# Performance work log

Hardware: AMD Instinct MI355X
Metric: run time of the kernel (lower is better)

The kernel has to match this reference:

```python
import jax, jax.numpy as jnp
import numpy as np

N, E, G = 50000, 800000, 128
IN, HID, OUT, H = 128, 64, 32, 4
EPS = 1e-5


def _bn(x, g, b, m, v):
    # BatchNorm1d in eval mode: normalize with running stats
    return (x - m) * jax.lax.rsqrt(v + EPS) * g + b


def _gat(x, src, dst, W, att_src, att_dst, bias, n):
    # PyG GATConv, concat=False: mean over heads
    h = (x @ W).reshape(n, H, -1)                      # [N,H,C]
    a_src = (h * att_src).sum(-1)                      # [N,H]
    a_dst = (h * att_dst).sum(-1)                      # [N,H]
    e = jax.nn.leaky_relu(a_src[src] + a_dst[dst], 0.2)  # [E,H]
    m = jax.ops.segment_max(e, dst, num_segments=n)    # segment softmax over incoming edges
    e = jnp.exp(e - m[dst])
    s = jax.ops.segment_sum(e, dst, num_segments=n)
    alpha = e / s[dst]                                  # [E,H]
    out = jax.ops.segment_sum(alpha[:, :, None] * h[src], dst, num_segments=n)  # [N,H,C]
    return out.mean(axis=1) + bias


def setup_inputs() -> dict:
    key = jax.random.key(0)
    ks = jax.random.split(key, 20)
    d = {
        "x": jax.random.normal(ks[0], (N, IN), jnp.float32),
        "edge_index": jax.random.randint(ks[1], (2, E), 0, N),
        "batch": jnp.sort(jax.random.randint(ks[2], (N,), 0, G)),
        # input_norm
        "in_gamma": jax.random.normal(ks[3], (IN,)) * 0.05 + 1.0,
        "in_beta": jax.random.normal(ks[4], (IN,)) * 0.05,
        "in_mean": jax.random.normal(ks[5], (IN,)) * 0.05,
        "in_var": jax.random.uniform(ks[6], (IN,)) + 0.5,
        # gat1
        "W1": jax.random.normal(ks[7], (IN, H * HID)) * (1.0 / np.sqrt(IN)),
        "as1": jax.random.normal(ks[8], (H, HID)) * 0.1,
        "ad1": jax.random.normal(ks[9], (H, HID)) * 0.1,
        "b1": jnp.zeros((HID,)),
        "bn1_g": jnp.ones((HID,)),
        "bn1_b": jnp.zeros((HID,)),
        "bn1_m": jax.random.normal(ks[10], (HID,)) * 0.05,
        "bn1_v": jax.random.uniform(ks[11], (HID,)) + 0.5,
        # gat2
        "W2": jax.random.normal(ks[12], (HID, H * HID)) * (1.0 / np.sqrt(HID)),
        "as2": jax.random.normal(ks[13], (H, HID)) * 0.1,
        "ad2": jax.random.normal(ks[14], (H, HID)) * 0.1,
        "b2": jnp.zeros((HID,)),
        "bn2_g": jnp.ones((HID,)),
        "bn2_b": jnp.zeros((HID,)),
        "bn2_m": jax.random.normal(ks[15], (HID,)) * 0.05,
        "bn2_v": jax.random.uniform(ks[16], (HID,)) + 0.5,
        # head
        "fc1_w": jax.random.normal(ks[17], (HID, HID // 2)) * (1.0 / np.sqrt(HID)),
        "fc1_b": jnp.zeros((HID // 2,)),
        "fc2_w": jax.random.normal(ks[18], (HID // 2, OUT)) * (1.0 / np.sqrt(HID // 2)),
        "fc2_b": jnp.zeros((OUT,)),
    }
    return d


def reference(x, edge_index, batch, in_gamma, in_beta, in_mean, in_var,
              W1, as1, ad1, b1, bn1_g, bn1_b, bn1_m, bn1_v,
              W2, as2, ad2, b2, bn2_g, bn2_b, bn2_m, bn2_v,
              fc1_w, fc1_b, fc2_w, fc2_b):
    n = x.shape[0]
    # PyG GATConv adds self-loops by default
    loop = jnp.arange(n)
    src = jnp.concatenate([edge_index[0], loop])
    dst = jnp.concatenate([edge_index[1], loop])

    h = _bn(x, in_gamma, in_beta, in_mean, in_var)
    h = _gat(h, src, dst, W1, as1, ad1, b1, n)
    h = jax.nn.relu(_bn(h, bn1_g, bn1_b, bn1_m, bn1_v))
    # dropout p=0.3 is identity in eval mode
    h = _gat(h, src, dst, W2, as2, ad2, b2, n)
    h = jax.nn.relu(_bn(h, bn2_g, bn2_b, bn2_m, bn2_v))

    # global mean pool over graphs
    sums = jax.ops.segment_sum(h, batch, num_segments=G)
    cnts = jax.ops.segment_sum(jnp.ones((n,), h.dtype), batch, num_segments=G)
    emb = sums / jnp.maximum(cnts, 1.0)[:, None]

    out = jax.nn.relu(emb @ fc1_w + fc1_b)
    return out @ fc2_w + fc2_b
```

## Files before the change

### kernel.cpp

```cpp
#include <hip/hip_runtime.h>
#include <hip/hip_bf16.h>

#define EPS   1e-5f
#define NH    4
#define DIN   128
#define DHID  64
#define DOUT  32
#define PNODES 256
#define CAP   128
#define GM    32

typedef __attribute__((ext_vector_type(8))) short short8;
typedef __attribute__((ext_vector_type(4))) float f32x4;

__device__ __forceinline__ float us2f(unsigned short u) {
    return __uint_as_float((unsigned)u << 16);
}
__device__ __forceinline__ unsigned short f2us(float v) {
    __hip_bfloat16 hb = __float2bfloat16(v);
    return *(unsigned short*)&hb;
}
__device__ __forceinline__ float lrelu(float a) { return (a >= 0.f) ? a : 0.2f * a; }

__global__ void k_init0(int* __restrict__ deg, float* __restrict__ pool, int N, int npool) {
    int g = blockIdx.x * blockDim.x + threadIdx.x;
    if (g < N) deg[g] = 1;
    if (g < npool) pool[g] = 0.f;
}

__global__ void k_hist(const int* __restrict__ ei, int* __restrict__ deg, int E) {
    int e = blockIdx.x * blockDim.x + threadIdx.x;
    if (e < E) atomicAdd(&deg[ei[E + e]], 1);
}

__global__ __launch_bounds__(256) void k_scan_a(const int* __restrict__ deg,
                                                int* __restrict__ rowptr,
                                                int* __restrict__ bsum, int N) {
    __shared__ int sh[256];
    const int t = threadIdx.x;
    const int i = blockIdx.x * 256 + t;
    int v = (i < N) ? deg[i] : 0;
    sh[t] = v;
    __syncthreads();
    #pragma unroll
    for (int o = 1; o < 256; o <<= 1) {
        int u = (t >= o) ? sh[t - o] : 0;
        __syncthreads();
        sh[t] += u;
        __syncthreads();
    }
    if (i < N) rowptr[i] = sh[t] - v;
    if (t == 255) bsum[blockIdx.x] = sh[255];
}

__global__ __launch_bounds__(256) void k_scan_b(int* __restrict__ bsum, int nb) {
    __shared__ int sh[256];
    const int t = threadIdx.x;
    int v = (t < nb) ? bsum[t] : 0;
    sh[t] = v;
    __syncthreads();
    #pragma unroll
    for (int o = 1; o < 256; o <<= 1) {
        int u = (t >= o) ? sh[t - o] : 0;
        __syncthreads();
        sh[t] += u;
        __syncthreads();
    }
    if (t < nb) bsum[t] = sh[t] - v;
}

__global__ __launch_bounds__(256) void k_scan_c(int* __restrict__ rowptr,
                                                int* __restrict__ cursor,
                                                const int* __restrict__ bsum,
                                                int N, int Etot) {
    const int i = blockIdx.x * 256 + threadIdx.x;
    if (i < N) {
        int v = rowptr[i] + bsum[blockIdx.x];
        rowptr[i] = v;
        cursor[i] = v;
    }
    if (i == 0) rowptr[N] = Etot;
}

__global__ void k_fill(const int* __restrict__ ei, int* __restrict__ cursor,
                       int* __restrict__ col, int E, int N) {
    int g = blockIdx.x * blockDim.x + threadIdx.x;
    if (g >= E + N) return;
    int s, d;
    if (g < E) { s = ei[g]; d = ei[E + g]; } else { s = d = g - E; }
    int pos = atomicAdd(&cursor[d], 1);
    col[pos] = s;
}

__global__ __launch_bounds__(256) void k_prep(
    const float* __restrict__ x,
    const float* __restrict__ ing, const float* __restrict__ inb,
    const float* __restrict__ inm, const float* __restrict__ inv,
    const float* __restrict__ W1, const float* __restrict__ W2,
    const float* __restrict__ as1, const float* __restrict__ ad1,
    const float* __restrict__ as2, const float* __restrict__ ad2,
    const float* __restrict__ b1,
    const float* __restrict__ bn1g, const float* __restrict__ bn1b,
    const float* __restrict__ bn1m, const float* __restrict__ bn1v,
    unsigned short* __restrict__ A, unsigned short* __restrict__ Wt,
    unsigned short* __restrict__ Wt2,
    unsigned short* __restrict__ Wast1, unsigned short* __restrict__ Wast2,
    float* __restrict__ scl1, float* __restrict__ shf1, int N)
{
    int g = blockIdx.x * blockDim.x + threadIdx.x;
    int totA = N * (DIN / 4);
    if (g < totA) {
        int n = g >> 5, k4 = (g & 31) * 4;
        float4 xv = *(const float4*)(x + (size_t)n * DIN + k4);
        float4 gm = *(const float4*)(ing + k4);
        float4 bb = *(const float4*)(inb + k4);
        float4 mm = *(const float4*)(inm + k4);
        float4 vv = *(const float4*)(inv + k4);
        ushort4 o;
        o.x = f2us((xv.x - mm.x) * rsqrtf(vv.x + EPS) * gm.x + bb.x);
        o.y = f2us((xv.y - mm.y) * rsqrtf(vv.y + EPS) * gm.y + bb.y);
        o.z = f2us((xv.z - mm.z) * rsqrtf(vv.z + EPS) * gm.z + bb.z);
        o.w = f2us((xv.w - mm.w) * rsqrtf(vv.w + EPS) * gm.w + bb.w);
        *(ushort4*)(A + (size_t)n * DIN + k4) = o;
    }
    if (g < 256 * DIN) {
        int n = g >> 7, k = g & 127;
        Wt[g] = f2us(W1[(size_t)k * 256 + n]);
    }
    if (g < 256 * DHID) {
        int n = g >> 6, k = g & 63;
        Wt2[g] = f2us(W2[(size_t)k * 256 + n]);
    }
    if (g < 16 * DIN) {
        int c = g >> 7, k = g & 127;
        float s = 0.f;
        if (c < 4)      { for (int j = 0; j < 64; ++j) s += W1[(size_t)k * 256 + c * 64 + j] * as1[c * 64 + j]; }
        else if (c < 8) { for (int j = 0; j < 64; ++j) s += W1[(size_t)k * 256 + (c - 4) * 64 + j] * ad1[(c - 4) * 64 + j]; }
        Wast1[g] = f2us(s);
    }
    if (g < 16 * DHID) {
        int c = g >> 6, k = g & 63;
        float s = 0.f;
        if (c < 4)      { for (int j = 0; j < 64; ++j) s += W2[(size_t)k * 256 + c * 64 + j] * as2[c * 64 + j]; }
        else if (c < 8) { for (int j = 0; j < 64; ++j) s += W2[(size_t)k * 256 + (c - 4) * 64 + j] * ad2[(c - 4) * 64 + j]; }
        Wast2[g] = f2us(s);
    }
    if (g < DHID) {
        float sc = bn1g[g] * rsqrtf(bn1v[g] + EPS);
        scl1[g] = sc;
        shf1[g] = (b1[g] - bn1m[g]) * sc + bn1b[g];
    }
}

__global__ __launch_bounds__(256) void k_att(
    const unsigned short* __restrict__ A,
    const unsigned short* __restrict__ Wast,
    float* __restrict__ asrc, float* __restrict__ adst, int K, int N)
{
    const int t = threadIdx.x;
    const int lane = t & 63, wv = t >> 6;
    const int qm = lane & 15, qd = lane >> 4;
    const int rowbase = blockIdx.x * 64 + wv * 16;

    int node = rowbase + qm;
    if (node >= N) node = N - 1;
    const unsigned short* ap = A + (size_t)node * K + qd * 8;
    const unsigned short* bp = Wast + (size_t)qm * K + qd * 8;

    f32x4 acc = (f32x4){0.f, 0.f, 0.f, 0.f};
    for (int ks = 0; ks < K / 32; ++ks) {
        short8 af = *(const short8*)(ap + ks * 32);
        short8 bf = *(const short8*)(bp + ks * 32);
        acc = __builtin_amdgcn_mfma_f32_16x16x32_bf16(af, bf, acc, 0, 0, 0);
    }
    const int c = qm;
    #pragma unroll
    for (int rg = 0; rg < 4; ++rg) {
        int nd = rowbase + qd * 4 + rg;
        if (nd < N) {
            if (c < 4)      asrc[nd * 4 + c] = acc[rg];
            else if (c < 8) adst[nd * 4 + (c - 4)] = acc[rg];
        }
    }
}

__global__ __launch_bounds__(256) void k_gemm1(
    const unsigned short* __restrict__ A,
    const unsigned short* __restrict__ Wt,
    __hip_bfloat16* __restrict__ h, int N)
{
    __shared__ float Csh[GM][260];
    const int t = threadIdx.x;
    const int lane = t & 63, wv = t >> 6;
    const int qm = lane & 15, qd = lane >> 4;
    const int base = blockIdx.x * GM;

    short8 afr[2][4];
    #pragma unroll
    for (int rt = 0; rt < 2; ++rt) {
        int node = base + rt * 16 + qm;
        if (node >= N) node = N - 1;
        const unsigned short* ap = A + (size_t)node * DIN + qd * 8;
        #pragma unroll
        for (int ks = 0; ks < 4; ++ks)
            afr[rt][ks] = *(const short8*)(ap + ks * 32);
    }

    const int n0 = wv * 64;
    f32x4 acc[2][4];
    #pragma unroll
    for (int rt = 0; rt < 2; ++rt)
        #pragma unroll
        for (int ct = 0; ct < 4; ++ct)
            acc[rt][ct] = (f32x4){0.f, 0.f, 0.f, 0.f};

    #pragma unroll
    for (int ct = 0; ct < 4; ++ct) {
        const unsigned short* bp = Wt + (size_t)(n0 + ct * 16 + qm) * DIN + qd * 8;
        #pragma unroll
        for (int ks = 0; ks < 4; ++ks) {
            short8 bfr = *(const short8*)(bp + ks * 32);
            acc[0][ct] = __builtin_amdgcn_mfma_f32_16x16x32_bf16(afr[0][ks], bfr, acc[0][ct], 0, 0, 0);
            acc[1][ct] = __builtin_amdgcn_mfma_f32_16x16x32_bf16(afr[1][ks], bfr, acc[1][ct], 0, 0, 0);
        }
    }

    #pragma unroll
    for (int rt = 0; rt < 2; ++rt)
        #pragma unroll
        for (int ct = 0; ct < 4; ++ct)
            #pragma unroll
            for (int rg = 0; rg < 4; ++rg)
                Csh[rt * 16 + qd * 4 + rg][n0 + ct * 16 + qm] = acc[rt][ct][rg];
    __syncthreads();

    const int hcol = ((t & 3) << 6) | (t >> 2);
    for (int r = 0; r < GM; ++r) {
        int node = base + r;
        if (node >= N) break;
        h[(size_t)node * 256 + t] = __float2bfloat16(Csh[r][hcol]);
    }
}

__global__ __launch_bounds__(256) void k_gemm2(
    const unsigned short* __restrict__ A2,
    const unsigned short* __restrict__ Wt2,
    __hip_bfloat16* __restrict__ h, int N)
{
    __shared__ float Csh[GM][260];
    const int t = threadIdx.x;
    const int lane = t & 63, wv = t >> 6;
    const int qm = lane & 15, qd = lane >> 4;
    const int base = blockIdx.x * GM;

    short8 afr[2][2];
    #pragma unroll
    for (int rt = 0; rt < 2; ++rt) {
        int node = base + rt * 16 + qm;
        if (node >= N) node = N - 1;
        const unsigned short* ap = A2 + (size_t)node * DHID + qd * 8;
        #pragma unroll
        for (int ks = 0; ks < 2; ++ks)
            afr[rt][ks] = *(const short8*)(ap + ks * 32);
    }

    const int n0 = wv * 64;
    f32x4 acc[2][4];
    #pragma unroll
    for (int rt = 0; rt < 2; ++rt)
        #pragma unroll
        for (int ct = 0; ct < 4; ++ct)
            acc[rt][ct] = (f32x4){0.f, 0.f, 0.f, 0.f};

    #pragma unroll
    for (int ct = 0; ct < 4; ++ct) {
        const unsigned short* bp = Wt2 + (size_t)(n0 + ct * 16 + qm) * DHID + qd * 8;
        #pragma unroll
        for (int ks = 0; ks < 2; ++ks) {
            short8 bfr = *(const short8*)(bp + ks * 32);
            acc[0][ct] = __builtin_amdgcn_mfma_f32_16x16x32_bf16(afr[0][ks], bfr, acc[0][ct], 0, 0, 0);
            acc[1][ct] = __builtin_amdgcn_mfma_f32_16x16x32_bf16(afr[1][ks], bfr, acc[1][ct], 0, 0, 0);
        }
    }

    #pragma unroll
    for (int rt = 0; rt < 2; ++rt)
        #pragma unroll
        for (int ct = 0; ct < 4; ++ct)
            #pragma unroll
            for (int rg = 0; rg < 4; ++rg)
                Csh[rt * 16 + qd * 4 + rg][n0 + ct * 16 + qm] = acc[rt][ct][rg];
    __syncthreads();

    const int hcol = ((t & 3) << 6) | (t >> 2);
    for (int r = 0; r < GM; ++r) {
        int node = base + r;
        if (node >= N) break;
        h[(size_t)node * 256 + t] = __float2bfloat16(Csh[r][hcol]);
    }
}

__global__ __launch_bounds__(256) void k_agg(
    const int* __restrict__ rowptr, const int* __restrict__ col,
    const float* __restrict__ asrc, const float* __restrict__ adst,
    const __hip_bfloat16* __restrict__ h,
    float* __restrict__ outf, unsigned short* __restrict__ outb,
    const float* __restrict__ scl, const float* __restrict__ shf,
    int mode, int N)
{
    __shared__ float4 exs[4][CAP];
    __shared__ int    cols[4][CAP];
    const int lane = threadIdx.x & 63;
    const int wv   = threadIdx.x >> 6;
    const int d = (blockIdx.x << 2) + wv;
    if (d >= N) return;
    const int r0  = rowptr[d];
    const int deg = rowptr[d + 1] - r0;

    const float4 ad4 = ((const float4*)adst)[d];
    const float4* __restrict__ as4 = (const float4*)asrc;

    float sm0 = 0.f, sm1 = 0.f, sm2 = 0.f, sm3 = 0.f;
    for (int j = lane; j < deg; j += 64) {
        int s = col[r0 + j];
        float4 a = as4[s];
        float e0 = __expf(lrelu(a.x + ad4.x));
        float e1 = __expf(lrelu(a.y + ad4.y));
        float e2 = __expf(lrelu(a.z + ad4.z));
        float e3 = __expf(lrelu(a.w + ad4.w));
        if (j < CAP) { cols[wv][j] = s; exs[wv][j] = make_float4(e0, e1, e2, e3); }
        sm0 += e0; sm1 += e1; sm2 += e2; sm3 += e3;
    }
    #pragma unroll
    for (int o = 1; o < 64; o <<= 1) {
        sm0 += __shfl_xor(sm0, o, 64);
        sm1 += __shfl_xor(sm1, o, 64);
        sm2 += __shfl_xor(sm2, o, 64);
        sm3 += __shfl_xor(sm3, o, 64);
    }
    const float i0 = 0.25f / sm0, i1 = 0.25f / sm1, i2 = 0.25f / sm2, i3 = 0.25f / sm3;

    const ushort4* __restrict__ hv = (const ushort4*)h;
    float a0 = 0.f, a1 = 0.f, a2 = 0.f, a3 = 0.f;
    float b0 = 0.f, b1 = 0.f, b2 = 0.f, b3 = 0.f;
    if (deg <= CAP) {
        int j = 0;
        for (; j + 3 < deg; j += 4) {
            int sA = cols[wv][j],     sB = cols[wv][j + 1];
            int sC = cols[wv][j + 2], sD = cols[wv][j + 3];
            ushort4 vA = hv[(size_t)sA * 64 + lane];
            ushort4 vB = hv[(size_t)sB * 64 + lane];
            ushort4 vC = hv[(size_t)sC * 64 + lane];
            ushort4 vD = hv[(size_t)sD * 64 + lane];
            float4 wA = exs[wv][j],     wB = exs[wv][j + 1];
            float4 wC = exs[wv][j + 2], wD = exs[wv][j + 3];
            a0 += wA.x * us2f(vA.x); a1 += wA.y * us2f(vA.y);
            a2 += wA.z * us2f(vA.z); a3 += wA.w * us2f(vA.w);
            b0 += wB.x * us2f(vB.x); b1 += wB.y * us2f(vB.y);
            b2 += wB.z * us2f(vB.z); b3 += wB.w * us2f(vB.w);
            a0 += wC.x * us2f(vC.x); a1 += wC.y * us2f(vC.y);
            a2 += wC.z * us2f(vC.z); a3 += wC.w * us2f(vC.w);
            b0 += wD.x * us2f(vD.x); b1 += wD.y * us2f(vD.y);
            b2 += wD.z * us2f(vD.z); b3 += wD.w * us2f(vD.w);
        }
        for (; j < deg; ++j) {
            int s = cols[wv][j];
            ushort4 v = hv[(size_t)s * 64 + lane];
            float4 w = exs[wv][j];
            a0 += w.x * us2f(v.x); a1 += w.y * us2f(v.y);
            a2 += w.z * us2f(v.z); a3 += w.w * us2f(v.w);
        }
    } else {
        for (int j = 0; j < deg; ++j) {
            int s; float4 w;
            if (j < CAP) { s = cols[wv][j]; w = exs[wv][j]; }
            else {
                s = col[r0 + j];
                float4 a = as4[s];
                w.x = __expf(lrelu(a.x + ad4.x)); w.y = __expf(lrelu(a.y + ad4.y));
                w.z = __expf(lrelu(a.z + ad4.z)); w.w = __expf(lrelu(a.w + ad4.w));
            }
            ushort4 v = hv[(size_t)s * 64 + lane];
            a0 += w.x * us2f(v.x); a1 += w.y * us2f(v.y);
            a2 += w.z * us2f(v.z); a3 += w.w * us2f(v.w);
        }
    }
    float acc = (a0 + b0) * i0 + (a1 + b1) * i1 + (a2 + b2) * i2 + (a3 + b3) * i3;

    if (mode) {
        float v = fmaxf(acc * scl[lane] + shf[lane], 0.f);
        outb[(size_t)d * 64 + lane] = f2us(v);
    } else {
        outf[(size_t)d * 64 + lane] = acc;
    }
}

__global__ __launch_bounds__(256) void k_pool(
    const float* __restrict__ outacc,
    const float* __restrict__ b2_,
    const float* __restrict__ bg, const float* __restrict__ bb,
    const float* __restrict__ bm, const float* __restrict__ bv,
    const int* __restrict__ batch,
    float* __restrict__ pool, float* __restrict__ cnt, int N)
{
    const int lane = threadIdx.x & 63;
    const int wave = threadIdx.x >> 6;
    const int base = blockIdx.x * PNODES;
    int end = base + PNODES; if (end > N) end = N;

    const float scale = bg[lane] * rsqrtf(bv[lane] + EPS);
    const float shift = (b2_[lane] - bm[lane]) * scale + bb[lane];

    float acc = 0.f;
    int cur = -1, cl = 0;
    for (int n = base + wave; n < end; n += 4) {
        int gr = batch[n];
        if (gr != cur) {
            if (cur >= 0) {
                atomicAdd(&pool[cur * 64 + lane], acc);
                if (lane == 0) atomicAdd(&cnt[cur], (float)cl);
            }
            cur = gr; acc = 0.f; cl = 0;
        }
        float v = fmaxf(outacc[(size_t)n * 64 + lane] * scale + shift, 0.f);
        acc += v; ++cl;
    }
    if (cur >= 0) {
        atomicAdd(&pool[cur * 64 + lane], acc);
        if (lane == 0) atomicAdd(&cnt[cur], (float)cl);
    }
}

__global__ void k_head(const float* __restrict__ pool, const float* __restrict__ cnt,
                       const float* __restrict__ fc1w, const float* __restrict__ fc1b,
                       const float* __restrict__ fc2w, const float* __restrict__ fc2b,
                       float* __restrict__ out)
{
    int g = blockIdx.x;
    int t = threadIdx.x;
    __shared__ float emb[64];
    __shared__ float z1[32];
    float c = fmaxf(cnt[g], 1.0f);
    emb[t] = pool[g * 64 + t] / c;
    __syncthreads();
    if (t < 32) {
        float s = fc1b[t];
        for (int k = 0; k < 64; ++k) s += emb[k] * fc1w[k * 32 + t];
        z1[t] = fmaxf(s, 0.f);
    }
    __syncthreads();
    if (t < 32) {
        float o = fc2b[t];
        for (int j = 0; j < 32; ++j) o += z1[j] * fc2w[j * 32 + t];
        out[g * 32 + t] = o;
    }
}

extern "C" void kernel_launch(void* const* d_in, const int* in_sizes, int n_in,
                              void* d_out, int out_size, void* d_ws, size_t ws_size,
                              hipStream_t stream)
{
    const float* x    = (const float*)d_in[0];
    const int*   ei   = (const int*)d_in[1];
    const int*   batch= (const int*)d_in[2];
    const float* ing  = (const float*)d_in[3];
    const float* inb  = (const float*)d_in[4];
    const float* inm  = (const float*)d_in[5];
    const float* inv  = (const float*)d_in[6];
    const float* W1   = (const float*)d_in[7];
    const float* as1  = (const float*)d_in[8];
    const float* ad1  = (const float*)d_in[9];
    const float* b1   = (const float*)d_in[10];
    const float* bn1g = (const float*)d_in[11];
    const float* bn1b = (const float*)d_in[12];
    const float* bn1m = (const float*)d_in[13];
    const float* bn1v = (const float*)d_in[14];
    const float* W2   = (const float*)d_in[15];
    const float* as2  = (const float*)d_in[16];
    const float* ad2  = (const float*)d_in[17];
    const float* b2   = (const float*)d_in[18];
    const float* bn2g = (const float*)d_in[19];
    const float* bn2b = (const float*)d_in[20];
    const float* bn2m = (const float*)d_in[21];
    const float* bn2v = (const float*)d_in[22];
    const float* fc1w = (const float*)d_in[23];
    const float* fc1b = (const float*)d_in[24];
    const float* fc2w = (const float*)d_in[25];
    const float* fc2b = (const float*)d_in[26];

    const int N = in_sizes[0] / DIN;
    const int E = in_sizes[1] / 2;
    const int G = out_size / DOUT;
    const int Etot = E + N;

    __hip_bfloat16* h = (__hip_bfloat16*)d_ws;
    float* asrc   = (float*)(h + (size_t)N * 256);
    float* adst   = asrc + (size_t)N * NH;
    unsigned short* Wt    = (unsigned short*)(adst + (size_t)N * NH);
    unsigned short* Wt2   = Wt + 256 * DIN;
    unsigned short* Wast1 = Wt2 + 256 * DHID;
    unsigned short* Wast2 = Wast1 + 16 * DIN;
    float* scl1   = (float*)(Wast2 + 16 * DHID);
    float* shf1   = scl1 + DHID;
    float* outacc = shf1 + DHID;
    unsigned short* A  = (unsigned short*)outacc;
    unsigned short* A2 = (unsigned short*)outacc;
    int*   deg    = (int*)(outacc + (size_t)N * DHID);
    int*   rowptr = deg + N;
    int*   cursor = rowptr + N + 1;
    int*   col    = cursor + N;
    float* pool   = (float*)(col + Etot);
    float* cnt    = pool + (size_t)G * DHID;
    int*   bsum   = (int*)(cnt + G);

    const int npool = G * DHID + G;
    const int nScanBlk = (N + 255) / 256;
    dim3 b256(256);

    k_init0<<<(N + 255) / 256, b256, 0, stream>>>(deg, pool, N, npool);
    k_hist<<<(E + 255) / 256, b256, 0, stream>>>(ei, deg, E);
    k_scan_a<<<nScanBlk, b256, 0, stream>>>(deg, rowptr, bsum, N);
    k_scan_b<<<1, b256, 0, stream>>>(bsum, nScanBlk);
    k_scan_c<<<nScanBlk, b256, 0, stream>>>(rowptr, cursor, bsum, N, Etot);
    k_fill<<<(Etot + 255) / 256, b256, 0, stream>>>(ei, cursor, col, E, N);

    const int prepThreads = N * (DIN / 4);
    k_prep<<<(prepThreads + 255) / 256, b256, 0, stream>>>(
        x, ing, inb, inm, inv, W1, W2, as1, ad1, as2, ad2,
        b1, bn1g, bn1b, bn1m, bn1v,
        A, Wt, Wt2, Wast1, Wast2, scl1, shf1, N);

    k_gemm1<<<(N + GM - 1) / GM, b256, 0, stream>>>(A, Wt, h, N);
    k_att<<<(N + 63) / 64, b256, 0, stream>>>(A, Wast1, asrc, adst, DIN, N);
    k_agg<<<(N + 3) / 4, b256, 0, stream>>>(rowptr, col, asrc, adst, h,
                                            (float*)nullptr, A2, scl1, shf1, 1, N);

    k_gemm2<<<(N + GM - 1) / GM, b256, 0, stream>>>(A2, Wt2, h, N);
    k_att<<<(N + 63) / 64, b256, 0, stream>>>(A2, Wast2, asrc, adst, DHID, N);
    k_agg<<<(N + 3) / 4, b256, 0, stream>>>(rowptr, col, asrc, adst, h,
                                            outacc, (unsigned short*)nullptr,
                                            (const float*)nullptr, (const float*)nullptr, 0, N);

    k_pool<<<(N + PNODES - 1) / PNODES, b256, 0, stream>>>(outacc, b2, bn2g, bn2b, bn2m, bn2v,
                                                           batch, pool, cnt, N);
    k_head<<<G, 64, 0, stream>>>(pool, cnt, fc1w, fc1b, fc2w, fc2b, (float*)d_out);
}
```

Baseline: 424.7 us.

## Store projected features as FP8 and fuse attention logits into GEMMs

The per-head projected features h are now stored as FP8 e4m3 instead of bf16, which halves the bytes gathered per edge in the aggregation kernels. The aggregation decodes them with packed fp8-to-f32 conversions. The separate attention-logit kernel is removed, and its MFMA is folded into each GEMM kernel, which reuses the A fragments already in registers. This saves a launch and a reread of the activations, at the cost of coarser feature precision that may exceed the accuracy tolerance.

```diff
diff --git a/kernel.cpp b/kernel.cpp
--- a/kernel.cpp
+++ b/kernel.cpp
@@ -12,6 +12,7 @@
 
 typedef __attribute__((ext_vector_type(8))) short short8;
 typedef __attribute__((ext_vector_type(4))) float f32x4;
+typedef __attribute__((ext_vector_type(2))) float f32x2;
 
 __device__ __forceinline__ float us2f(unsigned short u) {
     return __uint_as_float((unsigned)u << 16);
@@ -19,6 +20,10 @@
 __device__ __forceinline__ unsigned short f2us(float v) {
     __hip_bfloat16 hb = __float2bfloat16(v);
     return *(unsigned short*)&hb;
+}
+__device__ __forceinline__ unsigned char f2e4m3(float v) {
+    int p = __builtin_amdgcn_cvt_pk_fp8_f32(v, 0.f, 0, false);
+    return (unsigned char)(p & 0xff);
 }
 __device__ __forceinline__ float lrelu(float a) { return (a >= 0.f) ? a : 0.2f * a; }
 
@@ -152,42 +157,12 @@
     }
 }
 
-__global__ __launch_bounds__(256) void k_att(
-    const unsigned short* __restrict__ A,
-    const unsigned short* __restrict__ Wast,
-    float* __restrict__ asrc, float* __restrict__ adst, int K, int N)
-{
-    const int t = threadIdx.x;
-    const int lane = t & 63, wv = t >> 6;
-    const int qm = lane & 15, qd = lane >> 4;
-    const int rowbase = blockIdx.x * 64 + wv * 16;
-
-    int node = rowbase + qm;
-    if (node >= N) node = N - 1;
-    const unsigned short* ap = A + (size_t)node * K + qd * 8;
-    const unsigned short* bp = Wast + (size_t)qm * K + qd * 8;
-
-    f32x4 acc = (f32x4){0.f, 0.f, 0.f, 0.f};
-    for (int ks = 0; ks < K / 32; ++ks) {
-        short8 af = *(const short8*)(ap + ks * 32);
-        short8 bf = *(const short8*)(bp + ks * 32);
-        acc = __builtin_amdgcn_mfma_f32_16x16x32_bf16(af, bf, acc, 0, 0, 0);
-    }
-    const int c = qm;
-    #pragma unroll
-    for (int rg = 0; rg < 4; ++rg) {
-        int nd = rowbase + qd * 4 + rg;
-        if (nd < N) {
-            if (c < 4)      asrc[nd * 4 + c] = acc[rg];
-            else if (c < 8) adst[nd * 4 + (c - 4)] = acc[rg];
-        }
-    }
-}
-
 __global__ __launch_bounds__(256) void k_gemm1(
     const unsigned short* __restrict__ A,
     const unsigned short* __restrict__ Wt,
-    __hip_bfloat16* __restrict__ h, int N)
+    const unsigned short* __restrict__ Wast,
+    unsigned char* __restrict__ h,
+    float* __restrict__ asrc, float* __restrict__ adst, int N)
 {
     __shared__ float Csh[GM][260];
     const int t = threadIdx.x;
@@ -225,6 +200,30 @@
         }
     }
 
+    {
+        const unsigned short* wp = Wast + (size_t)qm * DIN + qd * 8;
+        f32x4 aat[2];
+        aat[0] = (f32x4){0.f, 0.f, 0.f, 0.f};
+        aat[1] = (f32x4){0.f, 0.f, 0.f, 0.f};
+        #pragma unroll
+        for (int ks = 0; ks < 4; ++ks) {
+            short8 wfr = *(const short8*)(wp + ks * 32);
+            aat[0] = __builtin_amdgcn_mfma_f32_16x16x32_bf16(afr[0][ks], wfr, aat[0], 0, 0, 0);
+            aat[1] = __builtin_amdgcn_mfma_f32_16x16x32_bf16(afr[1][ks], wfr, aat[1], 0, 0, 0);
+        }
+        const int c = qm;
+        #pragma unroll
+        for (int rt = 0; rt < 2; ++rt)
+            #pragma unroll
+            for (int rg = 0; rg < 4; ++rg) {
+                int nd = base + rt * 16 + qd * 4 + rg;
+                if (nd < N) {
+                    if (c < 4)      asrc[nd * 4 + c] = aat[rt][rg];
+                    else if (c < 8) adst[nd * 4 + (c - 4)] = aat[rt][rg];
+                }
+            }
+    }
+
     #pragma unroll
     for (int rt = 0; rt < 2; ++rt)
         #pragma unroll
@@ -238,14 +237,16 @@
     for (int r = 0; r < GM; ++r) {
         int node = base + r;
         if (node >= N) break;
-        h[(size_t)node * 256 + t] = __float2bfloat16(Csh[r][hcol]);
+        h[(size_t)node * 256 + t] = f2e4m3(Csh[r][hcol]);
     }
 }
 
 __global__ __launch_bounds__(256) void k_gemm2(
     const unsigned short* __restrict__ A2,
     const unsigned short* __restrict__ Wt2,
-    __hip_bfloat16* __restrict__ h, int N)
+    const unsigned short* __restrict__ Wast,
+    unsigned char* __restrict__ h,
+    float* __restrict__ asrc, float* __restrict__ adst, int N)
 {
     __shared__ float Csh[GM][260];
     const int t = threadIdx.x;
@@ -283,6 +284,30 @@
         }
     }
 
+    {
+        const unsigned short* wp = Wast + (size_t)qm * DHID + qd * 8;
+        f32x4 aat[2];
+        aat[0] = (f32x4){0.f, 0.f, 0.f, 0.f};
+        aat[1] = (f32x4){0.f, 0.f, 0.f, 0.f};
+        #pragma unroll
+        for (int ks = 0; ks < 2; ++ks) {
+            short8 wfr = *(const short8*)(wp + ks * 32);
+            aat[0] = __builtin_amdgcn_mfma_f32_16x16x32_bf16(afr[0][ks], wfr, aat[0], 0, 0, 0);
+            aat[1] = __builtin_amdgcn_mfma_f32_16x16x32_bf16(afr[1][ks], wfr, aat[1], 0, 0, 0);
+        }
+        const int c = qm;
+        #pragma unroll
+        for (int rt = 0; rt < 2; ++rt)
+            #pragma unroll
+            for (int rg = 0; rg < 4; ++rg) {
+                int nd = base + rt * 16 + qd * 4 + rg;
+                if (nd < N) {
+                    if (c < 4)      asrc[nd * 4 + c] = aat[rt][rg];
+                    else if (c < 8) adst[nd * 4 + (c - 4)] = aat[rt][rg];
+                }
+            }
+    }
+
     #pragma unroll
     for (int rt = 0; rt < 2; ++rt)
         #pragma unroll
@@ -296,14 +321,14 @@
     for (int r = 0; r < GM; ++r) {
         int node = base + r;
         if (node >= N) break;
-        h[(size_t)node * 256 + t] = __float2bfloat16(Csh[r][hcol]);
+        h[(size_t)node * 256 + t] = f2e4m3(Csh[r][hcol]);
     }
 }
 
 __global__ __launch_bounds__(256) void k_agg(
     const int* __restrict__ rowptr, const int* __restrict__ col,
     const float* __restrict__ asrc, const float* __restrict__ adst,
-    const __hip_bfloat16* __restrict__ h,
+    const unsigned char* __restrict__ h8,
     float* __restrict__ outf, unsigned short* __restrict__ outb,
     const float* __restrict__ scl, const float* __restrict__ shf,
     int mode, int N)
@@ -340,7 +365,7 @@
     }
     const float i0 = 0.25f / sm0, i1 = 0.25f / sm1, i2 = 0.25f / sm2, i3 = 0.25f / sm3;
 
-    const ushort4* __restrict__ hv = (const ushort4*)h;
+    const unsigned int* __restrict__ hu = (const unsigned int*)h8;
     float a0 = 0.f, a1 = 0.f, a2 = 0.f, a3 = 0.f;
     float b0 = 0.f, b1 = 0.f, b2 = 0.f, b3 = 0.f;
     if (deg <= CAP) {
@@ -348,27 +373,27 @@
         for (; j + 3 < deg; j += 4) {
             int sA = cols[wv][j],     sB = cols[wv][j + 1];
             int sC = cols[wv][j + 2], sD = cols[wv][j + 3];
-            ushort4 vA = hv[(size_t)sA * 64 + lane];
-            ushort4 vB = hv[(size_t)sB * 64 + lane];
-            ushort4 vC = hv[(size_t)sC * 64 + lane];
-            ushort4 vD = hv[(size_t)sD * 64 + lane];
+            unsigned int vA = hu[(size_t)sA * 64 + lane];
+            unsigned int vB = hu[(size_t)sB * 64 + lane];
+            unsigned int vC = hu[(size_t)sC * 64 + lane];
+            unsigned int vD = hu[(size_t)sD * 64 + lane];
             float4 wA = exs[wv][j],     wB = exs[wv][j + 1];
             float4 wC = exs[wv][j + 2], wD = exs[wv][j + 3];
-            a0 += wA.x * us2f(vA.x); a1 += wA.y * us2f(vA.y);
-            a2 += wA.z * us2f(vA.z); a3 += wA.w * us2f(vA.w);
-            b0 += wB.x * us2f(vB.x); b1 += wB.y * us2f(vB.y);
-            b2 += wB.z * us2f(vB.z); b3 += wB.w * us2f(vB.w);
-            a0 += wC.x * us2f(vC.x); a1 += wC.y * us2f(vC.y);
-            a2 += wC.z * us2f(vC.z); a3 += wC.w * us2f(vC.w);
-            b0 += wD.x * us2f(vD.x); b1 += wD.y * us2f(vD.y);
-            b2 += wD.z * us2f(vD.z); b3 += wD.w * us2f(vD.w);
+            f32x2 lA = __builtin_amdgcn_cvt_pk_f32_fp8(vA, false), hA = __builtin_amdgcn_cvt_pk_f32_fp8(vA, true);
+            f32x2 lB = __builtin_amdgcn_cvt_pk_f32_fp8(vB, false), hB = __builtin_amdgcn_cvt_pk_f32_fp8(vB, true);
+            f32x2 lC = __builtin_amdgcn_cvt_pk_f32_fp8(vC, false), hC = __builtin_amdgcn_cvt_pk_f32_fp8(vC, true);
+            f32x2 lD = __builtin_amdgcn_cvt_pk_f32_fp8(vD, false), hD = __builtin_amdgcn_cvt_pk_f32_fp8(vD, true);
+            a0 += wA.x * lA.x; a1 += wA.y * lA.y; a2 += wA.z * hA.x; a3 += wA.w * hA.y;
+            b0 += wB.x * lB.x; b1 += wB.y * lB.y; b2 += wB.z * hB.x; b3 += wB.w * hB.y;
+            a0 += wC.x * lC.x; a1 += wC.y * lC.y; a2 += wC.z * hC.x; a3 += wC.w * hC.y;
+            b0 += wD.x * lD.x; b1 += wD.y * lD.y; b2 += wD.z * hD.x; b3 += wD.w * hD.y;
         }
         for (; j < deg; ++j) {
             int s = cols[wv][j];
-            ushort4 v = hv[(size_t)s * 64 + lane];
+            unsigned int v = hu[(size_t)s * 64 + lane];
             float4 w = exs[wv][j];
-            a0 += w.x * us2f(v.x); a1 += w.y * us2f(v.y);
-            a2 += w.z * us2f(v.z); a3 += w.w * us2f(v.w);
+            f32x2 lo = __builtin_amdgcn_cvt_pk_f32_fp8(v, false), hi = __builtin_amdgcn_cvt_pk_f32_fp8(v, true);
+            a0 += w.x * lo.x; a1 += w.y * lo.y; a2 += w.z * hi.x; a3 += w.w * hi.y;
         }
     } else {
         for (int j = 0; j < deg; ++j) {
@@ -380,9 +405,9 @@
                 w.x = __expf(lrelu(a.x + ad4.x)); w.y = __expf(lrelu(a.y + ad4.y));
                 w.z = __expf(lrelu(a.z + ad4.z)); w.w = __expf(lrelu(a.w + ad4.w));
             }
-            ushort4 v = hv[(size_t)s * 64 + lane];
-            a0 += w.x * us2f(v.x); a1 += w.y * us2f(v.y);
-            a2 += w.z * us2f(v.z); a3 += w.w * us2f(v.w);
+            unsigned int v = hu[(size_t)s * 64 + lane];
+            f32x2 lo = __builtin_amdgcn_cvt_pk_f32_fp8(v, false), hi = __builtin_amdgcn_cvt_pk_f32_fp8(v, true);
+            a0 += w.x * lo.x; a1 += w.y * lo.y; a2 += w.z * hi.x; a3 += w.w * hi.y;
         }
     }
     float acc = (a0 + b0) * i0 + (a1 + b1) * i1 + (a2 + b2) * i2 + (a3 + b3) * i3;
@@ -493,8 +518,8 @@
     const int G = out_size / DOUT;
     const int Etot = E + N;
 
-    __hip_bfloat16* h = (__hip_bfloat16*)d_ws;
-    float* asrc   = (float*)(h + (size_t)N * 256);
+    unsigned char* h8 = (unsigned char*)d_ws;
+    float* asrc   = (float*)(h8 + (size_t)N * 256);
     float* adst   = asrc + (size_t)N * NH;
     unsigned short* Wt    = (unsigned short*)(adst + (size_t)N * NH);
     unsigned short* Wt2   = Wt + 256 * DIN;
@@ -530,14 +555,12 @@
         b1, bn1g, bn1b, bn1m, bn1v,
         A, Wt, Wt2, Wast1, Wast2, scl1, shf1, N);
 
-    k_gemm1<<<(N + GM - 1) / GM, b256, 0, stream>>>(A, Wt, h, N);
-    k_att<<<(N + 63) / 64, b256, 0, stream>>>(A, Wast1, asrc, adst, DIN, N);
-    k_agg<<<(N + 3) / 4, b256, 0, stream>>>(rowptr, col, asrc, adst, h,
+    k_gemm1<<<(N + GM - 1) / GM, b256, 0, stream>>>(A, Wt, Wast1, h8, asrc, adst, N);
+    k_agg<<<(N + 3) / 4, b256, 0, stream>>>(rowptr, col, asrc, adst, h8,
                                             (float*)nullptr, A2, scl1, shf1, 1, N);
 
-    k_gemm2<<<(N + GM - 1) / GM, b256, 0, stream>>>(A2, Wt2, h, N);
-    k_att<<<(N + 63) / 64, b256, 0, stream>>>(A2, Wast2, asrc, adst, DHID, N);
-    k_agg<<<(N + 3) / 4, b256, 0, stream>>>(rowptr, col, asrc, adst, h,
+    k_gemm2<<<(N + GM - 1) / GM, b256, 0, stream>>>(A2, Wt2, Wast2, h8, asrc, adst, N);
+    k_agg<<<(N + 3) / 4, b256, 0, stream>>>(rowptr, col, asrc, adst, h8,
                                             outacc, (unsigned short*)nullptr,
                                             (const float*)nullptr, (const float*)nullptr, 0, N);
 
```

Result: faster. 374.8 us (-11.7%).
